# Kernel tuning notes

Hardware: AMD Instinct MI355X
Metric: run time of the kernel (lower is better)

Reference implementation:

```python
import jax, jax.numpy as jnp
import numpy as np

D_MODEL = 1024
D_HEAD = 64


def setup_inputs() -> dict:
    key = jax.random.key(0)
    k_x, k_q, k_k, k_v, k_o = jax.random.split(key, 5)
    scale = 1.0 / np.sqrt(D_MODEL)
    residual_stream = jax.random.normal(k_x, (4, 2048, D_MODEL), dtype=jnp.float32)
    Q = scale * jax.random.normal(k_q, (D_MODEL, D_HEAD), dtype=jnp.float32)
    K = scale * jax.random.normal(k_k, (D_MODEL, D_HEAD), dtype=jnp.float32)
    V = scale * jax.random.normal(k_v, (D_MODEL, D_HEAD), dtype=jnp.float32)
    O = scale * jax.random.normal(k_o, (D_MODEL, D_HEAD), dtype=jnp.float32)
    return {"residual_stream": residual_stream, "Q": Q, "K": K, "V": V, "O": O}


def reference(residual_stream, Q, K, V, O) -> jnp.ndarray:
    # queries/keys: [B, S, d_head]
    queries = jnp.einsum('bsd,dh->bsh', residual_stream, Q)
    keys = jnp.einsum('bsd,dh->bsh', residual_stream, K)
    # NOTE: original module applies NO 1/sqrt(d_head) scaling.
    pre_attention = jnp.einsum('bqh,bkh->bqk', queries, keys)  # [B, S, S]
    S = pre_attention.shape[-1]
    causal = jnp.tril(jnp.ones((S, S), dtype=bool))
    pre_attention = jnp.where(causal[None], pre_attention, -jnp.inf)
    attention = jax.nn.softmax(pre_attention, axis=-1)
    # x = residual @ V @ O^T : [B, S, d_model]
    x = jnp.einsum('bsd,dh,eh->bse', residual_stream, V, O)
    return jnp.einsum('bqk,bke->bqe', attention, x)
```

## Files before the change

kernel.cpp:

```cpp
#include <hip/hip_runtime.h>
#include <hip/hip_bf16.h>
#include <math.h>

#define BATCH 4
#define SEQ   2048
#define DM    1024
#define DH    64
#define NROWS (BATCH*SEQ)

typedef __hip_bfloat16 bf16;
typedef __attribute__((ext_vector_type(8))) short short8;
typedef __attribute__((ext_vector_type(8))) unsigned short ushortx8;
typedef __attribute__((ext_vector_type(4))) float floatx4;

__device__ __forceinline__ ushort f2bf(float f) {
    union { bf16 h; ushort u; } cv;
    cv.h = __float2bfloat16(f);
    return cv.u;
}
__device__ __forceinline__ float bf2f(ushort u) {
    union { unsigned int i; float f; } v; v.i = ((unsigned int)u) << 16; return v.f;
}

__global__ __launch_bounds__(256) void wprep_kernel(
    const float* __restrict__ Q, const float* __restrict__ K,
    const float* __restrict__ V, const float* __restrict__ O,
    ushort* __restrict__ WhT, ushort* __restrict__ WlT,
    ushort* __restrict__ Oh, ushort* __restrict__ Ol)
{
    int n = blockIdx.x;
    if (n < 192) {
        const float* W = (n < 64) ? Q : (n < 128) ? K : V;
        int c = n & 63;
        for (int k = threadIdx.x; k < DM; k += 256) {
            float w = W[k * DH + c];
            ushort hi = f2bf(w);
            WhT[n * DM + k] = hi;
            WlT[n * DM + k] = f2bf(w - bf2f(hi));
        }
    } else {
        int e0 = (n - 192) << 4;
        for (int idx = threadIdx.x; idx < 16 * DH; idx += 256) {
            int off = (e0 << 6) + idx;
            float w = O[off];
            ushort hi = f2bf(w);
            Oh[off] = hi;
            Ol[off] = f2bf(w - bf2f(hi));
        }
    }
}

__global__ __launch_bounds__(256) void qkv_part_kernel(
    const float* __restrict__ x, const ushort* __restrict__ WhT,
    const ushort* __restrict__ WlT, float* __restrict__ Cpart)
{
    __shared__ __align__(16) ushort Xs[2][32][34];
    __shared__ __align__(16) ushort Ws[2][192][34];
    int s0 = blockIdx.x * 32;
    int kb = blockIdx.y * 256;
    int t = threadIdx.x;
    int wave = t >> 6, lane = t & 63, m_ = lane & 15, qd = lane >> 4;
    const floatx4 z4 = {0.f, 0.f, 0.f, 0.f};
    floatx4 accq[2] = {z4, z4}, acck[2] = {z4, z4}, accv[2] = {z4, z4};
    int xr = t >> 3, xc = (t & 7) * 4;
    for (int k0 = 0; k0 < 256; k0 += 32) {
        float4 v = *(const float4*)&x[(size_t)(s0 + xr) * DM + kb + k0 + xc];
        ushort h0 = f2bf(v.x), h1 = f2bf(v.y), h2 = f2bf(v.z), h3 = f2bf(v.w);
        *(ushort4*)&Xs[0][xr][xc] = make_ushort4(h0, h1, h2, h3);
        *(ushort4*)&Xs[1][xr][xc] = make_ushort4(
            f2bf(v.x - bf2f(h0)), f2bf(v.y - bf2f(h1)),
            f2bf(v.z - bf2f(h2)), f2bf(v.w - bf2f(h3)));
        #pragma unroll
        for (int j = 0; j < 3; ++j) {
            int idx = t + j * 256, n = idx >> 2, kc = (idx & 3) * 8;
            *(uint4*)&Ws[0][n][kc] = *(const uint4*)&WhT[n * DM + kb + k0 + kc];
            *(uint4*)&Ws[1][n][kc] = *(const uint4*)&WlT[n * DM + kb + k0 + kc];
        }
        __syncthreads();
        short8 ah[2], al[2];
        #pragma unroll
        for (int mi = 0; mi < 2; ++mi) {
            ah[mi] = *(const short8*)&Xs[0][mi * 16 + m_][qd * 8];
            al[mi] = *(const short8*)&Xs[1][mi * 16 + m_][qd * 8];
        }
        int nq = wave * 16 + m_, nk = 64 + wave * 16 + m_, nv = 128 + wave * 16 + m_;
        short8 bqh = *(const short8*)&Ws[0][nq][qd * 8];
        short8 bql = *(const short8*)&Ws[1][nq][qd * 8];
        short8 bkh = *(const short8*)&Ws[0][nk][qd * 8];
        short8 bkl = *(const short8*)&Ws[1][nk][qd * 8];
        short8 bvh = *(const short8*)&Ws[0][nv][qd * 8];
        #pragma unroll
        for (int mi = 0; mi < 2; ++mi) {
            accq[mi] = __builtin_amdgcn_mfma_f32_16x16x32_bf16(ah[mi], bqh, accq[mi], 0, 0, 0);
            accq[mi] = __builtin_amdgcn_mfma_f32_16x16x32_bf16(al[mi], bqh, accq[mi], 0, 0, 0);
            accq[mi] = __builtin_amdgcn_mfma_f32_16x16x32_bf16(ah[mi], bql, accq[mi], 0, 0, 0);
            acck[mi] = __builtin_amdgcn_mfma_f32_16x16x32_bf16(ah[mi], bkh, acck[mi], 0, 0, 0);
            acck[mi] = __builtin_amdgcn_mfma_f32_16x16x32_bf16(al[mi], bkh, acck[mi], 0, 0, 0);
            acck[mi] = __builtin_amdgcn_mfma_f32_16x16x32_bf16(ah[mi], bkl, acck[mi], 0, 0, 0);
            accv[mi] = __builtin_amdgcn_mfma_f32_16x16x32_bf16(ah[mi], bvh, accv[mi], 0, 0, 0);
        }
        __syncthreads();
    }
    float* Cp = Cpart + (size_t)blockIdx.y * (NROWS * 192);
    #pragma unroll
    for (int mi = 0; mi < 2; ++mi) {
        #pragma unroll
        for (int r = 0; r < 4; ++r) {
            int row = s0 + mi * 16 + qd * 4 + r;
            float* base = Cp + (size_t)row * 192;
            base[wave * 16 + m_]       = accq[mi][r];
            base[64 + wave * 16 + m_]  = acck[mi][r];
            base[128 + wave * 16 + m_] = accv[mi][r];
        }
    }
}

__global__ __launch_bounds__(256) void qkv_reduce_kernel(
    const float* __restrict__ Cpart,
    ushort* __restrict__ qh, ushort* __restrict__ ql,
    ushort* __restrict__ kh, ushort* __restrict__ kl, ushort* __restrict__ xvP)
{
    __shared__ ushort xvs[32][72];
    const size_t SL = (size_t)NROWS * 192;
    int row0 = blockIdx.x * 32;
    int t = threadIdx.x;
    #pragma unroll
    for (int i = 0; i < 24; ++i) {
        int e = i * 256 + t;
        int r = e / 192, c = e - r * 192;
        size_t row = row0 + r;
        size_t off = row * 192 + c;
        float s = Cpart[off] + Cpart[SL + off] + Cpart[2 * SL + off] + Cpart[3 * SL + off];
        ushort hi = f2bf(s);
        if (c < 64) {
            qh[row * 64 + c] = hi; ql[row * 64 + c] = f2bf(s - bf2f(hi));
        } else if (c < 128) {
            kh[row * 64 + c - 64] = hi; kl[row * 64 + c - 64] = f2bf(s - bf2f(hi));
        } else {
            xvs[r][c - 128] = hi;
        }
    }
    __syncthreads();
    int h = t & 63, qd = t >> 6;
    ushortx8 v;
    #pragma unroll
    for (int j = 0; j < 8; ++j)
        v[j] = xvs[4 * qd + (j & 3) + ((j >> 2) << 4)][h];
    int b = row0 >> 11, c32 = (row0 & 2047) >> 5;
    *(ushortx8*)&xvP[((((size_t)b << 6) + c32) * 4 + qd) * 512 + h * 8] = v;
}

__global__ __launch_bounds__(512) void attn_kernel(
    const ushort* __restrict__ qh, const ushort* __restrict__ ql,
    const ushort* __restrict__ kh, const ushort* __restrict__ kl,
    const ushort* __restrict__ xvP,
    const ushort* __restrict__ Oh, const ushort* __restrict__ Ol,
    float* __restrict__ out)
{
    __shared__ __align__(16) ushort Qs[2][2][16][72];
    __shared__ float LO[2][2][16][68];
    __shared__ float lred[8][2][16];
    __shared__ float lsc[2][16];
    int pp = blockIdx.x & 63, b = blockIdx.x >> 6;
    int srowA = pp << 4, srowB = (127 - pp) << 4;
    int t = threadIdx.x, wave = t >> 6, lane = t & 63, m_ = lane & 15, qd = lane >> 4;
    {
        int tile = t >> 8, hl = (t >> 7) & 1, r = (t >> 3) & 15, c = (t & 7) * 8;
        const ushort* src = (hl ? ql : qh) + (size_t)((b << 11) + (tile ? srowB : srowA) + r) * 64 + c;
        *(uint4*)&Qs[tile][hl][r][c] = *(const uint4*)src;
    }
    __syncthreads();
    int nA = (pp >> 2) + 1, nB = ((127 - pp) >> 2) + 1;
    int M = nA + nB;
    const ushort* khb = kh + (((size_t)b << 11)) * 64;
    const ushort* klb = kl + (((size_t)b << 11)) * 64;
    const ushort* xvb = xvP + ((size_t)b << 17);
    const floatx4 z4 = {0.f, 0.f, 0.f, 0.f};
    floatx4 accOA[4] = {z4, z4, z4, z4};
    floatx4 accOB[4] = {z4, z4, z4, z4};
    float llA = 0.f, llB = 0.f;
    for (int it = wave; it < M; it += 8) {
        int tile = (it >= nA);
        int c = tile ? (it - nA) : it;
        int srow = tile ? srowB : srowA;
        int k0 = c << 6;
        floatx4 accS[4] = {z4, z4, z4, z4};
        #pragma unroll
        for (int kk = 0; kk < 2; ++kk) {
            short8 bqh, bql;
            if (tile == 0) {
                bqh = *(const short8*)&Qs[0][0][m_][kk * 32 + qd * 8];
                bql = *(const short8*)&Qs[0][1][m_][kk * 32 + qd * 8];
            } else {
                bqh = *(const short8*)&Qs[1][0][m_][kk * 32 + qd * 8];
                bql = *(const short8*)&Qs[1][1][m_][kk * 32 + qd * 8];
            }
            #pragma unroll
            for (int mt = 0; mt < 4; ++mt) {
                size_t koff = (size_t)(k0 + mt * 16 + m_) * 64 + kk * 32 + qd * 8;
                short8 akh = *(const short8*)&khb[koff];
                short8 akl = *(const short8*)&klb[koff];
                accS[mt] = __builtin_amdgcn_mfma_f32_16x16x32_bf16(akh, bqh, accS[mt], 0, 0, 0);
                accS[mt] = __builtin_amdgcn_mfma_f32_16x16x32_bf16(akl, bqh, accS[mt], 0, 0, 0);
                accS[mt] = __builtin_amdgcn_mfma_f32_16x16x32_bf16(akh, bql, accS[mt], 0, 0, 0);
            }
        }
        int qrow = srow + m_;
        float lsum = 0.f;
        short8 pa[2];
        #pragma unroll
        for (int h2 = 0; h2 < 2; ++h2) {
            #pragma unroll
            for (int tt = 0; tt < 2; ++tt) {
                int mt = h2 * 2 + tt;
                #pragma unroll
                for (int r = 0; r < 4; ++r) {
                    int kc = k0 + mt * 16 + qd * 4 + r;
                    float p = (kc <= qrow) ? __expf(accS[mt][r]) : 0.f;
                    lsum += p;
                    pa[h2][tt * 4 + r] = (short)f2bf(p);
                }
            }
        }
        if (tile == 0) llA += lsum; else llB += lsum;
        #pragma unroll
        for (int h2 = 0; h2 < 2; ++h2) {
            int c32 = (k0 >> 5) + h2;
            const ushort* xb = xvb + ((size_t)c32 * 4 + qd) * 512 + m_ * 8;
            short8 x0 = *(const short8*)&xb[0];
            short8 x1 = *(const short8*)&xb[128];
            short8 x2 = *(const short8*)&xb[256];
            short8 x3 = *(const short8*)&xb[384];
            if (tile == 0) {
                accOA[0] = __builtin_amdgcn_mfma_f32_16x16x32_bf16(pa[h2], x0, accOA[0], 0, 0, 0);
                accOA[1] = __builtin_amdgcn_mfma_f32_16x16x32_bf16(pa[h2], x1, accOA[1], 0, 0, 0);
                accOA[2] = __builtin_amdgcn_mfma_f32_16x16x32_bf16(pa[h2], x2, accOA[2], 0, 0, 0);
                accOA[3] = __builtin_amdgcn_mfma_f32_16x16x32_bf16(pa[h2], x3, accOA[3], 0, 0, 0);
            } else {
                accOB[0] = __builtin_amdgcn_mfma_f32_16x16x32_bf16(pa[h2], x0, accOB[0], 0, 0, 0);
                accOB[1] = __builtin_amdgcn_mfma_f32_16x16x32_bf16(pa[h2], x1, accOB[1], 0, 0, 0);
                accOB[2] = __builtin_amdgcn_mfma_f32_16x16x32_bf16(pa[h2], x2, accOB[2], 0, 0, 0);
                accOB[3] = __builtin_amdgcn_mfma_f32_16x16x32_bf16(pa[h2], x3, accOB[3], 0, 0, 0);
            }
        }
    }
    llA += __shfl_xor(llA, 16); llA += __shfl_xor(llA, 32);
    llB += __shfl_xor(llB, 16); llB += __shfl_xor(llB, 32);
    if (qd == 0) { lred[wave][0][m_] = llA; lred[wave][1][m_] = llB; }
    int part = wave >> 2, w4 = wave & 3;
    for (int w = 0; w < 4; ++w) {
        if (w4 == w) {
            #pragma unroll
            for (int hn = 0; hn < 4; ++hn)
                #pragma unroll
                for (int r = 0; r < 4; ++r) {
                    int q = qd * 4 + r, h = hn * 16 + m_;
                    if (w == 0) {
                        LO[part][0][q][h] = accOA[hn][r];
                        LO[part][1][q][h] = accOB[hn][r];
                    } else {
                        LO[part][0][q][h] += accOA[hn][r];
                        LO[part][1][q][h] += accOB[hn][r];
                    }
                }
        }
        __syncthreads();
    }
    if (t < 32) {
        int tile = t >> 4, q = t & 15;
        float lt = 0.f;
        #pragma unroll
        for (int w = 0; w < 8; ++w) lt += lred[w][tile][q];
        lsc[tile][q] = 1.f / lt;
    }
    __syncthreads();
    int e0w = wave << 7;
    short8 Ah[2][2], Al[2][2];
    #pragma unroll
    for (int tile = 0; tile < 2; ++tile) {
        float sc = lsc[tile][m_];
        #pragma unroll
        for (int kk = 0; kk < 2; ++kk) {
            #pragma unroll
            for (int j = 0; j < 8; ++j) {
                int h = kk * 32 + qd * 8 + j;
                float v = (LO[0][tile][m_][h] + LO[1][tile][m_][h]) * sc;
                ushort hv = f2bf(v);
                Ah[tile][kk][j] = (short)hv;
                Al[tile][kk][j] = (short)f2bf(v - bf2f(hv));
            }
        }
    }
    floatx4 accE[2][8];
    #pragma unroll
    for (int tile = 0; tile < 2; ++tile)
        #pragma unroll
        for (int ni = 0; ni < 8; ++ni) accE[tile][ni] = z4;
    #pragma unroll
    for (int ni = 0; ni < 8; ++ni) {
        #pragma unroll
        for (int kk = 0; kk < 2; ++kk) {
            size_t boff = (size_t)(e0w + ni * 16 + m_) * 64 + kk * 32 + qd * 8;
            short8 bh = *(const short8*)&Oh[boff];
            short8 bl = *(const short8*)&Ol[boff];
            #pragma unroll
            for (int tile = 0; tile < 2; ++tile) {
                accE[tile][ni] = __builtin_amdgcn_mfma_f32_16x16x32_bf16(Ah[tile][kk], bh, accE[tile][ni], 0, 0, 0);
                accE[tile][ni] = __builtin_amdgcn_mfma_f32_16x16x32_bf16(Al[tile][kk], bh, accE[tile][ni], 0, 0, 0);
                accE[tile][ni] = __builtin_amdgcn_mfma_f32_16x16x32_bf16(Ah[tile][kk], bl, accE[tile][ni], 0, 0, 0);
            }
        }
    }
    float* ob = out + ((size_t)b * SEQ) * DM;
    #pragma unroll
    for (int tile = 0; tile < 2; ++tile) {
        int srow = tile ? srowB : srowA;
        #pragma unroll
        for (int r = 0; r < 4; ++r) {
            float* orow = ob + (size_t)(srow + qd * 4 + r) * DM + e0w;
            #pragma unroll
            for (int ni = 0; ni < 8; ++ni)
                orow[ni * 16 + m_] = accE[tile][ni][r];
        }
    }
}

extern "C" void kernel_launch(void* const* d_in, const int* in_sizes, int n_in,
                              void* d_out, int out_size, void* d_ws, size_t ws_size,
                              hipStream_t stream) {
    const float* x = (const float*)d_in[0];
    const float* Q = (const float*)d_in[1];
    const float* K = (const float*)d_in[2];
    const float* V = (const float*)d_in[3];
    const float* O = (const float*)d_in[4];
    float* out = (float*)d_out;

    char* ws = (char*)d_ws;
    ushort* qh   = (ushort*)(ws);
    ushort* ql   = (ushort*)(ws + (1ull  << 20));
    ushort* kh   = (ushort*)(ws + (2ull  << 20));
    ushort* kl   = (ushort*)(ws + (3ull  << 20));
    ushort* xvP  = (ushort*)(ws + (4ull  << 20));
    ushort* WhT  = (ushort*)(ws + (5ull  << 20));
    ushort* WlT  = (ushort*)(ws + (5ull  << 20) + (512ull << 10));
    ushort* Oh   = (ushort*)(ws + (6ull  << 20));
    ushort* Ol   = (ushort*)(ws + (6ull  << 20) + (128ull << 10));
    float*  Cpart = (float*)(ws + (23ull << 20));

    wprep_kernel<<<256, 256, 0, stream>>>(Q, K, V, O, WhT, WlT, Oh, Ol);
    qkv_part_kernel<<<dim3(NROWS / 32, 4), 256, 0, stream>>>(x, WhT, WlT, Cpart);
    qkv_reduce_kernel<<<NROWS / 32, 256, 0, stream>>>(Cpart, qh, ql, kh, kl, xvP);
    attn_kernel<<<64 * BATCH, 512, 0, stream>>>(qh, ql, kh, kl, xvP, Oh, Ol, out);
}
```

Before: 158.8 us.

## Stage K and XV tiles through double-buffered LDS with async global-to-LDS loads

The attention loop now stages each 64-key chunk of K hi/lo and XV into double-buffered shared memory using global_load_lds, with an XOR swizzle on K rows, prefetching the next chunk while the current one is computed. Work is split so each wave owns one query tile, a 32-key half of each chunk and half of the head dims, instead of waves striding over chunks with direct global loads. Q fragments are held in registers and the cross-wave reduction shrinks. The aim is to cut redundant global traffic and hide load latency. In exchange the loop runs nB iterations with a block-wide barrier each time, so the waves on the shorter tile sit idle during the extra iterations.

```diff
diff --git a/kernel.cpp b/kernel.cpp
--- a/kernel.cpp
+++ b/kernel.cpp
@@ -20,6 +20,12 @@
 }
 __device__ __forceinline__ float bf2f(ushort u) {
     union { unsigned int i; float f; } v; v.i = ((unsigned int)u) << 16; return v.f;
+}
+
+__device__ __forceinline__ void load_lds16(const ushort* g, ushort* l) {
+    __builtin_amdgcn_global_load_lds(
+        (const __attribute__((address_space(1))) unsigned int*)g,
+        (__attribute__((address_space(3))) unsigned int*)l, 16, 0, 0);
 }
 
 __global__ __launch_bounds__(256) void wprep_kernel(
@@ -157,145 +163,136 @@
     const ushort* __restrict__ Oh, const ushort* __restrict__ Ol,
     float* __restrict__ out)
 {
-    __shared__ __align__(16) ushort Qs[2][2][16][72];
-    __shared__ float LO[2][2][16][68];
-    __shared__ float lred[8][2][16];
+    __shared__ __align__(16) ushort Kbuf[2][8192];
+    __shared__ __align__(16) ushort xvbuf[2][4096];
+    __shared__ float LO[2][16][68];
+    __shared__ float lred[2][2][16];
     __shared__ float lsc[2][16];
     int pp = blockIdx.x & 63, b = blockIdx.x >> 6;
     int srowA = pp << 4, srowB = (127 - pp) << 4;
     int t = threadIdx.x, wave = t >> 6, lane = t & 63, m_ = lane & 15, qd = lane >> 4;
-    {
-        int tile = t >> 8, hl = (t >> 7) & 1, r = (t >> 3) & 15, c = (t & 7) * 8;
-        const ushort* src = (hl ? ql : qh) + (size_t)((b << 11) + (tile ? srowB : srowA) + r) * 64 + c;
-        *(uint4*)&Qs[tile][hl][r][c] = *(const uint4*)src;
-    }
-    __syncthreads();
     int nA = (pp >> 2) + 1, nB = ((127 - pp) >> 2) + 1;
-    int M = nA + nB;
+    int tile = wave >> 2, h2 = (wave >> 1) & 1, nh = wave & 1;
+    int srow = tile ? srowB : srowA;
+    int nT = tile ? nB : nA;
     const ushort* khb = kh + (((size_t)b << 11)) * 64;
     const ushort* klb = kl + (((size_t)b << 11)) * 64;
-    const ushort* xvb = xvP + ((size_t)b << 17);
+    const ushort* xvPb = xvP + ((size_t)b << 17);
+    short8 bq[2][2];
+    {
+        size_t qr = (size_t)((b << 11) + srow + m_) * 64 + qd * 8;
+        bq[0][0] = *(const short8*)&qh[qr];
+        bq[0][1] = *(const short8*)&qh[qr + 32];
+        bq[1][0] = *(const short8*)&ql[qr];
+        bq[1][1] = *(const short8*)&ql[qr + 32];
+    }
+    int drow = lane >> 3;
+    int dlc = ((lane & 7) ^ drow) * 8;
+    #define AT_STAGE(cc, buf)                                                   \
+        { int k0r_ = (cc) << 6;                                                 \
+          _Pragma("unroll")                                                     \
+          for (int i_ = 0; i_ < 3; ++i_) {                                      \
+              int c_ = wave * 3 + i_;                                           \
+              if (c_ < 8)                                                       \
+                  load_lds16(khb + (size_t)(k0r_ + c_ * 8 + drow) * 64 + dlc,   \
+                             &Kbuf[buf][c_ * 512]);                             \
+              else if (c_ < 16)                                                 \
+                  load_lds16(klb + (size_t)(k0r_ + (c_ - 8) * 8 + drow) * 64 + dlc, \
+                             &Kbuf[buf][4096 + (c_ - 8) * 512]);                \
+              else                                                              \
+                  load_lds16(xvPb + (size_t)(cc) * 4096 + (c_ - 16) * 512 + lane * 8, \
+                             &xvbuf[buf][(c_ - 16) * 512]);                     \
+          } }
     const floatx4 z4 = {0.f, 0.f, 0.f, 0.f};
-    floatx4 accOA[4] = {z4, z4, z4, z4};
-    floatx4 accOB[4] = {z4, z4, z4, z4};
-    float llA = 0.f, llB = 0.f;
-    for (int it = wave; it < M; it += 8) {
-        int tile = (it >= nA);
-        int c = tile ? (it - nA) : it;
-        int srow = tile ? srowB : srowA;
-        int k0 = c << 6;
-        floatx4 accS[4] = {z4, z4, z4, z4};
-        #pragma unroll
-        for (int kk = 0; kk < 2; ++kk) {
-            short8 bqh, bql;
-            if (tile == 0) {
-                bqh = *(const short8*)&Qs[0][0][m_][kk * 32 + qd * 8];
-                bql = *(const short8*)&Qs[0][1][m_][kk * 32 + qd * 8];
-            } else {
-                bqh = *(const short8*)&Qs[1][0][m_][kk * 32 + qd * 8];
-                bql = *(const short8*)&Qs[1][1][m_][kk * 32 + qd * 8];
-            }
-            #pragma unroll
-            for (int mt = 0; mt < 4; ++mt) {
-                size_t koff = (size_t)(k0 + mt * 16 + m_) * 64 + kk * 32 + qd * 8;
-                short8 akh = *(const short8*)&khb[koff];
-                short8 akl = *(const short8*)&klb[koff];
-                accS[mt] = __builtin_amdgcn_mfma_f32_16x16x32_bf16(akh, bqh, accS[mt], 0, 0, 0);
-                accS[mt] = __builtin_amdgcn_mfma_f32_16x16x32_bf16(akl, bqh, accS[mt], 0, 0, 0);
-                accS[mt] = __builtin_amdgcn_mfma_f32_16x16x32_bf16(akh, bql, accS[mt], 0, 0, 0);
-            }
-        }
-        int qrow = srow + m_;
-        float lsum = 0.f;
-        short8 pa[2];
-        #pragma unroll
-        for (int h2 = 0; h2 < 2; ++h2) {
+    floatx4 accO[2] = {z4, z4};
+    float ll = 0.f;
+    int qrow = srow + m_;
+    AT_STAGE(0, 0)
+    for (int c = 0; c < nB; ++c) {
+        __syncthreads();
+        if (c + 1 < nB) AT_STAGE(c + 1, (c + 1) & 1)
+        if (c < nT) {
+            int bufi = c & 1;
+            floatx4 accS[2] = {z4, z4};
+            #pragma unroll
+            for (int kk = 0; kk < 2; ++kk) {
+                #pragma unroll
+                for (int tt = 0; tt < 2; ++tt) {
+                    int row = (2 * h2 + tt) * 16 + m_;
+                    int chunk = ((kk << 2) + qd) ^ (m_ & 7);
+                    const ushort* ph = &Kbuf[bufi][row * 64 + chunk * 8];
+                    short8 akh = *(const short8*)ph;
+                    short8 akl = *(const short8*)(ph + 4096);
+                    accS[tt] = __builtin_amdgcn_mfma_f32_16x16x32_bf16(akh, bq[0][kk], accS[tt], 0, 0, 0);
+                    accS[tt] = __builtin_amdgcn_mfma_f32_16x16x32_bf16(akl, bq[0][kk], accS[tt], 0, 0, 0);
+                    accS[tt] = __builtin_amdgcn_mfma_f32_16x16x32_bf16(akh, bq[1][kk], accS[tt], 0, 0, 0);
+                }
+            }
+            float lsum = 0.f;
+            short8 pa;
             #pragma unroll
             for (int tt = 0; tt < 2; ++tt) {
-                int mt = h2 * 2 + tt;
                 #pragma unroll
                 for (int r = 0; r < 4; ++r) {
-                    int kc = k0 + mt * 16 + qd * 4 + r;
-                    float p = (kc <= qrow) ? __expf(accS[mt][r]) : 0.f;
+                    int kc = c * 64 + (2 * h2 + tt) * 16 + qd * 4 + r;
+                    float p = (kc <= qrow) ? __expf(accS[tt][r]) : 0.f;
                     lsum += p;
-                    pa[h2][tt * 4 + r] = (short)f2bf(p);
+                    pa[tt * 4 + r] = (short)f2bf(p);
                 }
             }
-        }
-        if (tile == 0) llA += lsum; else llB += lsum;
-        #pragma unroll
-        for (int h2 = 0; h2 < 2; ++h2) {
-            int c32 = (k0 >> 5) + h2;
-            const ushort* xb = xvb + ((size_t)c32 * 4 + qd) * 512 + m_ * 8;
-            short8 x0 = *(const short8*)&xb[0];
-            short8 x1 = *(const short8*)&xb[128];
-            short8 x2 = *(const short8*)&xb[256];
-            short8 x3 = *(const short8*)&xb[384];
-            if (tile == 0) {
-                accOA[0] = __builtin_amdgcn_mfma_f32_16x16x32_bf16(pa[h2], x0, accOA[0], 0, 0, 0);
-                accOA[1] = __builtin_amdgcn_mfma_f32_16x16x32_bf16(pa[h2], x1, accOA[1], 0, 0, 0);
-                accOA[2] = __builtin_amdgcn_mfma_f32_16x16x32_bf16(pa[h2], x2, accOA[2], 0, 0, 0);
-                accOA[3] = __builtin_amdgcn_mfma_f32_16x16x32_bf16(pa[h2], x3, accOA[3], 0, 0, 0);
-            } else {
-                accOB[0] = __builtin_amdgcn_mfma_f32_16x16x32_bf16(pa[h2], x0, accOB[0], 0, 0, 0);
-                accOB[1] = __builtin_amdgcn_mfma_f32_16x16x32_bf16(pa[h2], x1, accOB[1], 0, 0, 0);
-                accOB[2] = __builtin_amdgcn_mfma_f32_16x16x32_bf16(pa[h2], x2, accOB[2], 0, 0, 0);
-                accOB[3] = __builtin_amdgcn_mfma_f32_16x16x32_bf16(pa[h2], x3, accOB[3], 0, 0, 0);
-            }
-        }
-    }
-    llA += __shfl_xor(llA, 16); llA += __shfl_xor(llA, 32);
-    llB += __shfl_xor(llB, 16); llB += __shfl_xor(llB, 32);
-    if (qd == 0) { lred[wave][0][m_] = llA; lred[wave][1][m_] = llB; }
-    int part = wave >> 2, w4 = wave & 3;
-    for (int w = 0; w < 4; ++w) {
-        if (w4 == w) {
-            #pragma unroll
-            for (int hn = 0; hn < 4; ++hn)
+            if (nh == 0) ll += lsum;
+            const ushort* Xb = &xvbuf[bufi][(h2 * 4 + qd) * 512];
+            #pragma unroll
+            for (int i = 0; i < 2; ++i) {
+                int h = (nh * 2 + i) * 16 + m_;
+                short8 xv = *(const short8*)&Xb[h * 8];
+                accO[i] = __builtin_amdgcn_mfma_f32_16x16x32_bf16(pa, xv, accO[i], 0, 0, 0);
+            }
+        }
+    }
+    ll += __shfl_xor(ll, 16); ll += __shfl_xor(ll, 32);
+    if (qd == 0 && nh == 0) lred[tile][h2][m_] = ll;
+    #pragma unroll
+    for (int h2r = 0; h2r < 2; ++h2r) {
+        if (h2 == h2r) {
+            #pragma unroll
+            for (int i = 0; i < 2; ++i)
                 #pragma unroll
                 for (int r = 0; r < 4; ++r) {
-                    int q = qd * 4 + r, h = hn * 16 + m_;
-                    if (w == 0) {
-                        LO[part][0][q][h] = accOA[hn][r];
-                        LO[part][1][q][h] = accOB[hn][r];
-                    } else {
-                        LO[part][0][q][h] += accOA[hn][r];
-                        LO[part][1][q][h] += accOB[hn][r];
-                    }
+                    int q = qd * 4 + r, h = (nh * 2 + i) * 16 + m_;
+                    if (h2r == 0) LO[tile][q][h] = accO[i][r];
+                    else          LO[tile][q][h] += accO[i][r];
                 }
         }
         __syncthreads();
     }
     if (t < 32) {
-        int tile = t >> 4, q = t & 15;
-        float lt = 0.f;
-        #pragma unroll
-        for (int w = 0; w < 8; ++w) lt += lred[w][tile][q];
-        lsc[tile][q] = 1.f / lt;
+        int tl = t >> 4, q = t & 15;
+        lsc[tl][q] = 1.f / (lred[tl][0][q] + lred[tl][1][q]);
     }
     __syncthreads();
     int e0w = wave << 7;
     short8 Ah[2][2], Al[2][2];
     #pragma unroll
-    for (int tile = 0; tile < 2; ++tile) {
-        float sc = lsc[tile][m_];
+    for (int tl = 0; tl < 2; ++tl) {
+        float sc = lsc[tl][m_];
         #pragma unroll
         for (int kk = 0; kk < 2; ++kk) {
             #pragma unroll
             for (int j = 0; j < 8; ++j) {
                 int h = kk * 32 + qd * 8 + j;
-                float v = (LO[0][tile][m_][h] + LO[1][tile][m_][h]) * sc;
+                float v = LO[tl][m_][h] * sc;
                 ushort hv = f2bf(v);
-                Ah[tile][kk][j] = (short)hv;
-                Al[tile][kk][j] = (short)f2bf(v - bf2f(hv));
+                Ah[tl][kk][j] = (short)hv;
+                Al[tl][kk][j] = (short)f2bf(v - bf2f(hv));
             }
         }
     }
     floatx4 accE[2][8];
     #pragma unroll
-    for (int tile = 0; tile < 2; ++tile)
-        #pragma unroll
-        for (int ni = 0; ni < 8; ++ni) accE[tile][ni] = z4;
+    for (int tl = 0; tl < 2; ++tl)
+        #pragma unroll
+        for (int ni = 0; ni < 8; ++ni) accE[tl][ni] = z4;
     #pragma unroll
     for (int ni = 0; ni < 8; ++ni) {
         #pragma unroll
@@ -304,25 +301,26 @@
             short8 bh = *(const short8*)&Oh[boff];
             short8 bl = *(const short8*)&Ol[boff];
             #pragma unroll
-            for (int tile = 0; tile < 2; ++tile) {
-                accE[tile][ni] = __builtin_amdgcn_mfma_f32_16x16x32_bf16(Ah[tile][kk], bh, accE[tile][ni], 0, 0, 0);
-                accE[tile][ni] = __builtin_amdgcn_mfma_f32_16x16x32_bf16(Al[tile][kk], bh, accE[tile][ni], 0, 0, 0);
-                accE[tile][ni] = __builtin_amdgcn_mfma_f32_16x16x32_bf16(Ah[tile][kk], bl, accE[tile][ni], 0, 0, 0);
+            for (int tl = 0; tl < 2; ++tl) {
+                accE[tl][ni] = __builtin_amdgcn_mfma_f32_16x16x32_bf16(Ah[tl][kk], bh, accE[tl][ni], 0, 0, 0);
+                accE[tl][ni] = __builtin_amdgcn_mfma_f32_16x16x32_bf16(Al[tl][kk], bh, accE[tl][ni], 0, 0, 0);
+                accE[tl][ni] = __builtin_amdgcn_mfma_f32_16x16x32_bf16(Ah[tl][kk], bl, accE[tl][ni], 0, 0, 0);
             }
         }
     }
     float* ob = out + ((size_t)b * SEQ) * DM;
     #pragma unroll
-    for (int tile = 0; tile < 2; ++tile) {
-        int srow = tile ? srowB : srowA;
+    for (int tl = 0; tl < 2; ++tl) {
+        int srw = tl ? srowB : srowA;
         #pragma unroll
         for (int r = 0; r < 4; ++r) {
-            float* orow = ob + (size_t)(srow + qd * 4 + r) * DM + e0w;
+            float* orow = ob + (size_t)(srw + qd * 4 + r) * DM + e0w;
             #pragma unroll
             for (int ni = 0; ni < 8; ++ni)
-                orow[ni * 16 + m_] = accE[tile][ni][r];
-        }
-    }
+                orow[ni * 16 + m_] = accE[tl][ni][r];
+        }
+    }
+    #undef AT_STAGE
 }
 
 extern "C" void kernel_launch(void* const* d_in, const int* in_sizes, int n_in,
```

Measured after the change: 164.6 us. +3.7%, slower.
